# Kernel tuning notes

Measured on AMD Instinct MI355X. Metric: run time of the kernel, lower is better.

The kernel has to match this reference:

```python
import jax, jax.numpy as jnp
import numpy as np

B, T, D, N = 32, 2048, 1024, 1024  # batch, time, feature dim, n_dense


def setup_inputs() -> dict:
    key = jax.random.key(0)
    ks = jax.random.split(key, 8)
    s = 1.0 / np.sqrt(D)
    return {
        "query": jax.random.normal(ks[0], (B, D), jnp.float32),
        "values": jax.random.normal(ks[1], (B, T, D), jnp.float32),
        "W1": jax.random.uniform(ks[2], (D, N), jnp.float32, -s, s),
        "b1": jnp.zeros((N,), jnp.float32),
        "W2": jax.random.uniform(ks[3], (D, N), jnp.float32, -s, s),
        "b2": jnp.zeros((N,), jnp.float32),
        "V": jax.random.uniform(ks[4], (N, 1), jnp.float32, -1.0 / np.sqrt(N), 1.0 / np.sqrt(N)),
        "bV": jnp.zeros((1,), jnp.float32),
    }


def reference(query, values, W1, b1, W2, b2, V, bV):
    # q_proj: [B, 1, N], v_proj: [B, T, N]
    q_proj = (query @ W1 + b1)[:, None, :]
    v_proj = jnp.einsum("btd,dn->btn", values, W2) + b2
    # score: [B, T, 1]
    score = jnp.tanh(q_proj + v_proj) @ V + bV
    attention_weights = jax.nn.softmax(score, axis=1)  # softmax over time
    # context: [B, D]
    context_vector = jnp.sum(attention_weights * values, axis=1)
    return (context_vector, attention_weights)
```

## Files before the change

kernel.cpp:

```cpp
#include <hip/hip_runtime.h>
#include <hip/hip_bf16.h>

#define B_ 32
#define T_ 2048
#define D_ 1024
#define N_ 1024
#define M_ (B_*T_)

#define BM 64
#define BN 128
#define BK 64

typedef short bf16x8 __attribute__((ext_vector_type(8)));
typedef float f32x4 __attribute__((ext_vector_type(4)));
typedef unsigned short us4 __attribute__((ext_vector_type(4)));

__device__ __forceinline__ unsigned short bf16_rn(float x) {
    unsigned u = __float_as_uint(x);
    u += 0x7FFFu + ((u >> 16) & 1u);
    return (unsigned short)(u >> 16);
}

__device__ __forceinline__ void gload_lds16(const void* g, void* l) {
    __builtin_amdgcn_global_load_lds(
        (__attribute__((address_space(1))) void*)(g),
        (__attribute__((address_space(3))) void*)(l), 16, 0, 0);
}

__global__ void k0_w2t(const float* __restrict__ W2,
                       unsigned short* __restrict__ Th) {
    __shared__ float tile[32][33];
    int n0 = blockIdx.x * 32, d0 = blockIdx.y * 32;
    int tx = threadIdx.x & 31, ty = threadIdx.x >> 5;
    #pragma unroll
    for (int i = 0; i < 4; i++) {
        int d = d0 + ty + i * 8;
        tile[ty + i * 8][tx] = W2[d * N_ + n0 + tx];
    }
    __syncthreads();
    #pragma unroll
    for (int i = 0; i < 4; i++) {
        int n = n0 + ty + i * 8;
        Th[n * D_ + d0 + tx] = bf16_rn(tile[tx][ty + i * 8]);
    }
}

__global__ void k1_qproj(const float* __restrict__ query,
                         const float* __restrict__ W1,
                         const float* __restrict__ b1,
                         float* __restrict__ qp) {
    int b = blockIdx.x;
    int n = blockIdx.y * 256 + threadIdx.x;
    const float* q = query + b * D_;
    const float* w = W1 + n;
    float s = 0.f;
    #pragma unroll 8
    for (int d = 0; d < D_; d++) s += q[d] * w[d * N_];
    qp[b * N_ + n] = s + b1[n];
}

template<bool USE_WS_A>
__global__ __launch_bounds__(256, 2) void k2_score(
    const float* __restrict__ values,
    const unsigned short* __restrict__ W2Th,
    const float* __restrict__ qp,
    const float* __restrict__ b2,
    const float* __restrict__ V,
    const float* __restrict__ bV,
    float* __restrict__ score,
    unsigned short* __restrict__ Ah) {
    __shared__ unsigned short sAh[BM * BK];
    __shared__ unsigned short sBh[BN * BK];
    __shared__ float red[2 * BM];

    const int tid = threadIdx.x;
    const int lane = tid & 63;
    const int wid = tid >> 6;
    const int wm = wid >> 1, wn = wid & 1;
    const int g = lane >> 4, c16 = lane & 15;

    const int m0 = blockIdx.x * BM;
    const int b = m0 >> 11;

    const int a_c4 = tid & 15;
    const int a_r0 = tid >> 4;
    const int b_rl = lane >> 3;
    const int b_j = lane & 7;

    float rowpart[8];
    #pragma unroll
    for (int i = 0; i < 8; i++) rowpart[i] = 0.f;

    for (int nt = 0; nt < N_ / BN; nt++) {
        f32x4 acc[2][4];
        #pragma unroll
        for (int mi = 0; mi < 2; mi++)
            #pragma unroll
            for (int ni = 0; ni < 4; ni++) {
                f32x4 z = {0.f, 0.f, 0.f, 0.f};
                acc[mi][ni] = z;
            }

        for (int kt = 0; kt < D_ / BK; kt++) {
            const int k0 = kt * BK;
            __syncthreads();

            #pragma unroll
            for (int i = 0; i < 4; i++) {
                int r = wid * 32 + i * 8 + b_rl;
                int jj = b_j ^ (r & 7);
                size_t soff = (size_t)(nt * BN + r) * D_ + k0 + jj * 8;
                gload_lds16(W2Th + soff, &sBh[(wid * 32 + i * 8) * 64]);
            }

            if (USE_WS_A && nt > 0) {
                #pragma unroll
                for (int i = 0; i < 2; i++) {
                    int r = wid * 16 + i * 8 + b_rl;
                    int jj = b_j ^ (r & 7);
                    size_t soff = (size_t)(m0 + r) * D_ + k0 + jj * 8;
                    gload_lds16(Ah + soff, &sAh[(wid * 16 + i * 8) * 64]);
                }
            } else {
                const float* abase = values + (size_t)m0 * D_ + k0;
                #pragma unroll
                for (int p = 0; p < 4; p++) {
                    int r = p * 16 + a_r0;
                    float4 v = *(const float4*)(abase + (size_t)r * D_ + a_c4 * 4);
                    float vv[4] = {v.x, v.y, v.z, v.w};
                    us4 hv;
                    #pragma unroll
                    for (int q = 0; q < 4; q++)
                        hv[q] = bf16_rn(vv[q]);
                    int idx = r * 64 + ((((a_c4 >> 1) ^ (r & 7)) << 3) | ((a_c4 & 1) << 2));
                    *(us4*)&sAh[idx] = hv;
                    if (USE_WS_A) {
                        size_t goff = (size_t)(m0 + r) * D_ + k0 + a_c4 * 4;
                        *(us4*)&Ah[goff] = hv;
                    }
                }
            }

            __syncthreads();

            #pragma unroll
            for (int s = 0; s < 2; s++) {
                bf16x8 aH[2], bH[4];
                #pragma unroll
                for (int mi = 0; mi < 2; mi++) {
                    int r = wm * 32 + mi * 16 + c16;
                    int idx = r * 64 + (((s * 4 + g) ^ (r & 7)) << 3);
                    aH[mi] = *(const bf16x8*)&sAh[idx];
                }
                #pragma unroll
                for (int ni = 0; ni < 4; ni++) {
                    int r = wn * 64 + ni * 16 + c16;
                    int idx = r * 64 + (((s * 4 + g) ^ (r & 7)) << 3);
                    bH[ni] = *(const bf16x8*)&sBh[idx];
                }
                #pragma unroll
                for (int mi = 0; mi < 2; mi++)
                    #pragma unroll
                    for (int ni = 0; ni < 4; ni++)
                        acc[mi][ni] = __builtin_amdgcn_mfma_f32_16x16x32_bf16(aH[mi], bH[ni], acc[mi][ni], 0, 0, 0);
            }
        }

        #pragma unroll
        for (int ni = 0; ni < 4; ni++) {
            int n = nt * BN + wn * 64 + ni * 16 + c16;
            float qv = qp[b * N_ + n] + b2[n];
            float Vv = V[n];
            #pragma unroll
            for (int mi = 0; mi < 2; mi++)
                #pragma unroll
                for (int r = 0; r < 4; r++) {
                    rowpart[mi * 4 + r] += tanhf(acc[mi][ni][r] + qv) * Vv;
                }
        }
    }

    #pragma unroll
    for (int i = 0; i < 8; i++) {
        float v = rowpart[i];
        v += __shfl_xor(v, 1);
        v += __shfl_xor(v, 2);
        v += __shfl_xor(v, 4);
        v += __shfl_xor(v, 8);
        rowpart[i] = v;
    }
    if (c16 == 0) {
        #pragma unroll
        for (int mi = 0; mi < 2; mi++)
            #pragma unroll
            for (int r = 0; r < 4; r++)
                red[wn * BM + wm * 32 + mi * 16 + g * 4 + r] = rowpart[mi * 4 + r];
    }
    __syncthreads();
    if (tid < BM) {
        score[m0 + tid] = red[tid] + red[BM + tid] + bV[0];
    }
}

__global__ void k3_softmax(float* __restrict__ sw) {
    int b = blockIdx.x;
    float* row = sw + b * T_;
    int tid = threadIdx.x;
    float v[8];
    float lmax = -1e30f;
    #pragma unroll
    for (int i = 0; i < 8; i++) {
        v[i] = row[tid + i * 256];
        lmax = fmaxf(lmax, v[i]);
    }
    #pragma unroll
    for (int d = 1; d < 64; d <<= 1) lmax = fmaxf(lmax, __shfl_xor(lmax, d));
    __shared__ float sm[4], ss[4];
    if ((tid & 63) == 0) sm[tid >> 6] = lmax;
    __syncthreads();
    lmax = fmaxf(fmaxf(sm[0], sm[1]), fmaxf(sm[2], sm[3]));
    float lsum = 0.f;
    #pragma unroll
    for (int i = 0; i < 8; i++) {
        v[i] = expf(v[i] - lmax);
        lsum += v[i];
    }
    #pragma unroll
    for (int d = 1; d < 64; d <<= 1) lsum += __shfl_xor(lsum, d);
    if ((tid & 63) == 0) ss[tid >> 6] = lsum;
    __syncthreads();
    lsum = ss[0] + ss[1] + ss[2] + ss[3];
    float inv = 1.f / lsum;
    #pragma unroll
    for (int i = 0; i < 8; i++) row[tid + i * 256] = v[i] * inv;
}

__global__ void k4_context(const float* __restrict__ values,
                           const float* __restrict__ w,
                           float* __restrict__ ctx) {
    int b = blockIdx.x;
    int dc = blockIdx.y;
    int tc = blockIdx.z;
    int d4 = threadIdx.x & 31;
    int th = threadIdx.x >> 5;
    const float* wrow = w + b * T_;
    int d = dc * 128 + d4 * 4;
    const float* vbase = values + (size_t)b * T_ * D_ + d;
    float4 acc = {0.f, 0.f, 0.f, 0.f};
    int t0 = tc * 256 + th * 32;
    for (int t = t0; t < t0 + 32; t++) {
        float wt = wrow[t];
        float4 vv = *(const float4*)(vbase + (size_t)t * D_);
        acc.x += wt * vv.x;
        acc.y += wt * vv.y;
        acc.z += wt * vv.z;
        acc.w += wt * vv.w;
    }
    __shared__ float4 red4[256];
    red4[threadIdx.x] = acc;
    __syncthreads();
    if (th == 0) {
        float4 s = red4[d4];
        #pragma unroll
        for (int i = 1; i < 8; i++) {
            float4 o = red4[i * 32 + d4];
            s.x += o.x; s.y += o.y; s.z += o.z; s.w += o.w;
        }
        atomicAdd(&ctx[b * D_ + d + 0], s.x);
        atomicAdd(&ctx[b * D_ + d + 1], s.y);
        atomicAdd(&ctx[b * D_ + d + 2], s.z);
        atomicAdd(&ctx[b * D_ + d + 3], s.w);
    }
}

extern "C" void kernel_launch(void* const* d_in, const int* in_sizes, int n_in,
                              void* d_out, int out_size, void* d_ws, size_t ws_size,
                              hipStream_t stream) {
    const float* query  = (const float*)d_in[0];
    const float* values = (const float*)d_in[1];
    const float* W1     = (const float*)d_in[2];
    const float* b1     = (const float*)d_in[3];
    const float* W2     = (const float*)d_in[4];
    const float* b2     = (const float*)d_in[5];
    const float* V      = (const float*)d_in[6];
    const float* bV     = (const float*)d_in[7];

    float* ctx = (float*)d_out;
    float* weights = (float*)d_out + B_ * D_;

    size_t need_base = (size_t)N_ * D_ * sizeof(unsigned short) + (size_t)B_ * N_ * sizeof(float);
    size_t need_full = need_base + (size_t)M_ * D_ * sizeof(unsigned short);
    if (ws_size < need_base) return;
    unsigned short* Th = (unsigned short*)d_ws;
    float* qp = (float*)(Th + (size_t)N_ * D_);
    unsigned short* Ahi = (unsigned short*)(qp + (size_t)B_ * N_);

    k0_w2t<<<dim3(N_ / 32, D_ / 32), 256, 0, stream>>>(W2, Th);
    k1_qproj<<<dim3(B_, N_ / 256), 256, 0, stream>>>(query, W1, b1, qp);
    if (ws_size >= need_full) {
        k2_score<true><<<M_ / BM, 256, 0, stream>>>(values, Th, qp, b2, V, bV, weights, Ahi);
    } else {
        k2_score<false><<<M_ / BM, 256, 0, stream>>>(values, Th, qp, b2, V, bV, weights, Ahi);
    }
    k3_softmax<<<B_, 256, 0, stream>>>(weights);
    hipMemsetAsync(ctx, 0, (size_t)B_ * D_ * sizeof(float), stream);
    k4_context<<<dim3(B_, 8, 8), 256, 0, stream>>>(values, weights, ctx);
}
```

Measured before the change: 381.2 us.

## Pre-convert values to bf16 in a separate pass and split score GEMM over N

Adds a standalone kernel that converts all of values to bf16 in workspace, so the score GEMM always loads A tiles with async global-to-LDS loads instead of converting fp32 inline on the first N tile. The score kernel grid gains a second dimension that splits the N tiles in two, doubling the block count, and the partial row sums are combined with atomicAdd into a pre-zeroed score buffer. The bV bias is dropped because a softmax over time is invariant to adding a constant. The cost is an extra full read and write pass over values, a memset, and atomics, and the kernel no longer runs at all when the workspace is too small.

```diff
diff --git a/kernel.cpp b/kernel.cpp
--- a/kernel.cpp
+++ b/kernel.cpp
@@ -10,6 +10,7 @@
 #define BM 64
 #define BN 128
 #define BK 64
+#define NTSPLIT 2
 
 typedef short bf16x8 __attribute__((ext_vector_type(8)));
 typedef float f32x4 __attribute__((ext_vector_type(4)));
@@ -42,6 +43,23 @@
     for (int i = 0; i < 4; i++) {
         int n = n0 + ty + i * 8;
         Th[n * D_ + d0 + tx] = bf16_rn(tile[tx][ty + i * 8]);
+    }
+}
+
+__global__ void k0_vals(const float* __restrict__ v,
+                        unsigned short* __restrict__ o) {
+    size_t i = ((size_t)blockIdx.x * 256 + threadIdx.x) * 8;
+    const size_t stride = (size_t)gridDim.x * 256 * 8;
+    for (; i < (size_t)M_ * D_; i += stride) {
+        float4 a = *(const float4*)(v + i);
+        float4 b = *(const float4*)(v + i + 4);
+        us4 h0, h1;
+        h0[0] = bf16_rn(a.x); h0[1] = bf16_rn(a.y);
+        h0[2] = bf16_rn(a.z); h0[3] = bf16_rn(a.w);
+        h1[0] = bf16_rn(b.x); h1[1] = bf16_rn(b.y);
+        h1[2] = bf16_rn(b.z); h1[3] = bf16_rn(b.w);
+        *(us4*)(o + i) = h0;
+        *(us4*)(o + i + 4) = h1;
     }
 }
 
@@ -59,16 +77,13 @@
     qp[b * N_ + n] = s + b1[n];
 }
 
-template<bool USE_WS_A>
 __global__ __launch_bounds__(256, 2) void k2_score(
-    const float* __restrict__ values,
+    const unsigned short* __restrict__ Av,
     const unsigned short* __restrict__ W2Th,
     const float* __restrict__ qp,
     const float* __restrict__ b2,
     const float* __restrict__ V,
-    const float* __restrict__ bV,
-    float* __restrict__ score,
-    unsigned short* __restrict__ Ah) {
+    float* __restrict__ score) {
     __shared__ unsigned short sAh[BM * BK];
     __shared__ unsigned short sBh[BN * BK];
     __shared__ float red[2 * BM];
@@ -81,9 +96,8 @@
 
     const int m0 = blockIdx.x * BM;
     const int b = m0 >> 11;
-
-    const int a_c4 = tid & 15;
-    const int a_r0 = tid >> 4;
+    const int nt0 = blockIdx.y * (N_ / BN / NTSPLIT);
+
     const int b_rl = lane >> 3;
     const int b_j = lane & 7;
 
@@ -91,7 +105,7 @@
     #pragma unroll
     for (int i = 0; i < 8; i++) rowpart[i] = 0.f;
 
-    for (int nt = 0; nt < N_ / BN; nt++) {
+    for (int nt = nt0; nt < nt0 + N_ / BN / NTSPLIT; nt++) {
         f32x4 acc[2][4];
         #pragma unroll
         for (int mi = 0; mi < 2; mi++)
@@ -112,33 +126,12 @@
                 size_t soff = (size_t)(nt * BN + r) * D_ + k0 + jj * 8;
                 gload_lds16(W2Th + soff, &sBh[(wid * 32 + i * 8) * 64]);
             }
-
-            if (USE_WS_A && nt > 0) {
-                #pragma unroll
-                for (int i = 0; i < 2; i++) {
-                    int r = wid * 16 + i * 8 + b_rl;
-                    int jj = b_j ^ (r & 7);
-                    size_t soff = (size_t)(m0 + r) * D_ + k0 + jj * 8;
-                    gload_lds16(Ah + soff, &sAh[(wid * 16 + i * 8) * 64]);
-                }
-            } else {
-                const float* abase = values + (size_t)m0 * D_ + k0;
-                #pragma unroll
-                for (int p = 0; p < 4; p++) {
-                    int r = p * 16 + a_r0;
-                    float4 v = *(const float4*)(abase + (size_t)r * D_ + a_c4 * 4);
-                    float vv[4] = {v.x, v.y, v.z, v.w};
-                    us4 hv;
-                    #pragma unroll
-                    for (int q = 0; q < 4; q++)
-                        hv[q] = bf16_rn(vv[q]);
-                    int idx = r * 64 + ((((a_c4 >> 1) ^ (r & 7)) << 3) | ((a_c4 & 1) << 2));
-                    *(us4*)&sAh[idx] = hv;
-                    if (USE_WS_A) {
-                        size_t goff = (size_t)(m0 + r) * D_ + k0 + a_c4 * 4;
-                        *(us4*)&Ah[goff] = hv;
-                    }
-                }
+            #pragma unroll
+            for (int i = 0; i < 2; i++) {
+                int r = wid * 16 + i * 8 + b_rl;
+                int jj = b_j ^ (r & 7);
+                size_t soff = (size_t)(m0 + r) * D_ + k0 + jj * 8;
+                gload_lds16(Av + soff, &sAh[(wid * 16 + i * 8) * 64]);
             }
 
             __syncthreads();
@@ -198,7 +191,7 @@
     }
     __syncthreads();
     if (tid < BM) {
-        score[m0 + tid] = red[tid] + red[BM + tid] + bV[0];
+        atomicAdd(&score[m0 + tid], red[tid] + red[BM + tid]);
     }
 }
 
@@ -283,25 +276,23 @@
     const float* W2     = (const float*)d_in[4];
     const float* b2     = (const float*)d_in[5];
     const float* V      = (const float*)d_in[6];
-    const float* bV     = (const float*)d_in[7];
 
     float* ctx = (float*)d_out;
     float* weights = (float*)d_out + B_ * D_;
 
-    size_t need_base = (size_t)N_ * D_ * sizeof(unsigned short) + (size_t)B_ * N_ * sizeof(float);
-    size_t need_full = need_base + (size_t)M_ * D_ * sizeof(unsigned short);
-    if (ws_size < need_base) return;
+    size_t need = (size_t)N_ * D_ * sizeof(unsigned short)
+                + (size_t)B_ * N_ * sizeof(float)
+                + (size_t)M_ * D_ * sizeof(unsigned short);
+    if (ws_size < need) return;
     unsigned short* Th = (unsigned short*)d_ws;
     float* qp = (float*)(Th + (size_t)N_ * D_);
-    unsigned short* Ahi = (unsigned short*)(qp + (size_t)B_ * N_);
+    unsigned short* Av = (unsigned short*)(qp + (size_t)B_ * N_);
 
     k0_w2t<<<dim3(N_ / 32, D_ / 32), 256, 0, stream>>>(W2, Th);
+    k0_vals<<<2048, 256, 0, stream>>>(values, Av);
     k1_qproj<<<dim3(B_, N_ / 256), 256, 0, stream>>>(query, W1, b1, qp);
-    if (ws_size >= need_full) {
-        k2_score<true><<<M_ / BM, 256, 0, stream>>>(values, Th, qp, b2, V, bV, weights, Ahi);
-    } else {
-        k2_score<false><<<M_ / BM, 256, 0, stream>>>(values, Th, qp, b2, V, bV, weights, Ahi);
-    }
+    hipMemsetAsync(weights, 0, (size_t)B_ * T_ * sizeof(float), stream);
+    k2_score<<<dim3(M_ / BM, NTSPLIT), 256, 0, stream>>>(Av, Th, qp, b2, V, weights);
     k3_softmax<<<B_, 256, 0, stream>>>(weights);
     hipMemsetAsync(ctx, 0, (size_t)B_ * D_ * sizeof(float), stream);
     k4_context<<<dim3(B_, 8, 8), 256, 0, stream>>>(values, weights, ctx);
```

Result: no change. 387.9 us (+1.8%).
